# Kernel tuning notes

Measured on AMD Instinct MI355X. Metric: run time of the kernel, lower is better.

## Reference

```python
import jax, jax.numpy as jnp
import numpy as np


def setup_inputs() -> dict:
    key = jax.random.key(0)
    k1, k2 = jax.random.split(key)
    B, T, D = 32, 512, 512
    encoder_output = jax.random.normal(k1, (B, T, D), dtype=jnp.float32)
    durations = jax.random.randint(k2, (B, T), 0, 8, dtype=jnp.int32)
    return {"encoder_output": encoder_output, "durations": durations, "t_out": 4096}


def reference(encoder_output, durations, t_out):
    # Faithful to the TF loop: duration = max(dur, 1); repeat each phoneme
    # vector `duration` times along time; pad to fixed length t_out with zeros.
    B, T, D = encoder_output.shape
    dur = jnp.maximum(durations.astype(jnp.int32), 1)        # [B, T]
    ends = jnp.cumsum(dur, axis=1)                            # [B, T] cumulative end frame per phoneme
    pos = jnp.arange(t_out, dtype=jnp.int32)                  # [t_out] output frame indices
    # For frame j, source phoneme = first t with ends[t] > j  (searchsorted right)
    idx = jax.vmap(lambda e: jnp.searchsorted(e, pos, side='right'))(ends)  # [B, t_out]
    valid = pos[None, :] < ends[:, -1:]                       # frames past total length -> zero pad
    idx = jnp.minimum(idx, T - 1)
    out = jnp.take_along_axis(encoder_output, idx[:, :, None], axis=1)      # [B, t_out, D]
    return out * valid[:, :, None].astype(encoder_output.dtype)
```

## Files before the change

### kernel.cpp

```cpp
#include <hip/hip_runtime.h>


#define T_PH 512
#define FPB  8

typedef float f32x4 __attribute__((ext_vector_type(4)));

__global__ __launch_bounds__(256) void lr_fused_kernel(
    const f32x4* __restrict__ enc,
    const int*   __restrict__ dur,
    f32x4*       __restrict__ out,
    int T, int t_out) {

    __shared__ int sp[T_PH / 2];
    __shared__ int e[T_PH];
    __shared__ int idx8[FPB];

    const int tid = threadIdx.x;
    const int b   = blockIdx.y;
    const int j0  = blockIdx.x * FPB;

    int2 d2 = ((const int2*)(dur + b * T))[tid];
    int v0 = (d2.x < 1) ? 1 : d2.x;
    int v1 = (d2.y < 1) ? 1 : d2.y;
    sp[tid] = v0 + v1;
    __syncthreads();

    for (int off = 1; off < T_PH / 2; off <<= 1) {
        int add = (tid >= off) ? sp[tid - off] : 0;
        __syncthreads();
        sp[tid] += add;
        __syncthreads();
    }
    int S = sp[tid];
    e[2 * tid]     = S - v1;
    e[2 * tid + 1] = S;
    __syncthreads();

    const int total = e[T_PH - 1];

    if (tid < FPB) {
        int j = j0 + tid;
        int r;
        if (j >= total) {
            r = -1;
        } else {
            int lo = 0, hi = T_PH - 1;
            while (lo < hi) {
                int mid = (lo + hi) >> 1;
                if (e[mid] <= j) lo = mid + 1; else hi = mid;
            }
            r = lo;
        }
        idx8[tid] = r;
    }
    __syncthreads();

    const int lane = tid & 127;
    const int fh   = tid >> 7;

    const f32x4* __restrict__ encb = enc + (size_t)b * T_PH * 128;
    f32x4* __restrict__ outb = out + ((size_t)b * t_out + j0) * 128 + lane;

    const f32x4 zero = {0.f, 0.f, 0.f, 0.f};

    int p0 = idx8[fh + 0];
    int p1 = idx8[fh + 2];
    int p2 = idx8[fh + 4];
    int p3 = idx8[fh + 6];

    f32x4 w0 = (p0 >= 0) ? encb[(size_t)p0 * 128 + lane] : zero;
    f32x4 w1 = (p1 >= 0) ? encb[(size_t)p1 * 128 + lane] : zero;
    f32x4 w2 = (p2 >= 0) ? encb[(size_t)p2 * 128 + lane] : zero;
    f32x4 w3 = (p3 >= 0) ? encb[(size_t)p3 * 128 + lane] : zero;

    __builtin_nontemporal_store(w0, &outb[(size_t)(fh + 0) * 128]);
    __builtin_nontemporal_store(w1, &outb[(size_t)(fh + 2) * 128]);
    __builtin_nontemporal_store(w2, &outb[(size_t)(fh + 4) * 128]);
    __builtin_nontemporal_store(w3, &outb[(size_t)(fh + 6) * 128]);
}

extern "C" void kernel_launch(void* const* d_in, const int* in_sizes, int n_in,
                              void* d_out, int out_size, void* d_ws, size_t ws_size,
                              hipStream_t stream) {
    const float* enc = (const float*)d_in[0];
    const int* dur   = (const int*)d_in[1];
    float* out       = (float*)d_out;

    const int BT = in_sizes[1];
    const int T  = T_PH;
    const int B  = BT / T;
    const int D  = in_sizes[0] / BT;
    const int t_out = out_size / (B * D);

    dim3 grid(t_out / FPB, B);
    lr_fused_kernel<<<grid, 256, 0, stream>>>(
        (const f32x4*)enc, dur, (f32x4*)out, T, t_out);
}
```

Baseline: 52.02 us.

## Use wavefront shuffle scan and double frames per block

Replaces the shared-memory Hillis-Steele prefix sum, which needs many __syncthreads barriers, with a wave-level shuffle scan plus a small cross-wave combine. Doubles frames per block from 8 to 16, so each block's redundant duration scan is spread over twice as much output. This halves the grid, and each thread now issues eight gather loads and eight streaming stores instead of four, which raises register use.

```diff
diff --git a/kernel.cpp b/kernel.cpp
--- a/kernel.cpp
+++ b/kernel.cpp
@@ -2,7 +2,7 @@
 
 
 #define T_PH 512
-#define FPB  8
+#define FPB  16
 
 typedef float f32x4 __attribute__((ext_vector_type(4)));
 
@@ -10,29 +10,36 @@
     const f32x4* __restrict__ enc,
     const int*   __restrict__ dur,
     f32x4*       __restrict__ out,
-    int T, int t_out) {
+    int t_out) {
 
-    __shared__ int sp[T_PH / 2];
     __shared__ int e[T_PH];
-    __shared__ int idx8[FPB];
+    __shared__ int wtot[4];
+    __shared__ int idxs[FPB];
 
-    const int tid = threadIdx.x;
-    const int b   = blockIdx.y;
-    const int j0  = blockIdx.x * FPB;
+    const int tid  = threadIdx.x;
+    const int wav  = tid >> 6;
+    const int lane = tid & 63;
+    const int b    = blockIdx.y;
+    const int j0   = blockIdx.x * FPB;
 
-    int2 d2 = ((const int2*)(dur + b * T))[tid];
+    int2 d2 = ((const int2*)(dur + b * T_PH))[tid];
     int v0 = (d2.x < 1) ? 1 : d2.x;
     int v1 = (d2.y < 1) ? 1 : d2.y;
-    sp[tid] = v0 + v1;
+    int p  = v0 + v1;
+
+    #pragma unroll
+    for (int off = 1; off < 64; off <<= 1) {
+        int t = __shfl_up(p, off);
+        if (lane >= off) p += t;
+    }
+    if (lane == 63) wtot[wav] = p;
     __syncthreads();
 
-    for (int off = 1; off < T_PH / 2; off <<= 1) {
-        int add = (tid >= off) ? sp[tid - off] : 0;
-        __syncthreads();
-        sp[tid] += add;
-        __syncthreads();
-    }
-    int S = sp[tid];
+    int wbase = 0;
+    #pragma unroll
+    for (int w = 0; w < 3; ++w)
+        wbase += (wav > w) ? wtot[w] : 0;
+    int S = wbase + p;
     e[2 * tid]     = S - v1;
     e[2 * tid + 1] = S;
     __syncthreads();
@@ -52,32 +59,30 @@
             }
             r = lo;
         }
-        idx8[tid] = r;
+        idxs[tid] = r;
     }
     __syncthreads();
 
-    const int lane = tid & 127;
-    const int fh   = tid >> 7;
+    const int lane128 = tid & 127;
+    const int fh      = tid >> 7;
 
     const f32x4* __restrict__ encb = enc + (size_t)b * T_PH * 128;
-    f32x4* __restrict__ outb = out + ((size_t)b * t_out + j0) * 128 + lane;
+    f32x4* __restrict__ outb = out + ((size_t)b * t_out + j0) * 128 + lane128;
 
     const f32x4 zero = {0.f, 0.f, 0.f, 0.f};
 
-    int p0 = idx8[fh + 0];
-    int p1 = idx8[fh + 2];
-    int p2 = idx8[fh + 4];
-    int p3 = idx8[fh + 6];
+    int pi[8];
+    #pragma unroll
+    for (int k = 0; k < 8; ++k) pi[k] = idxs[fh + 2 * k];
 
-    f32x4 w0 = (p0 >= 0) ? encb[(size_t)p0 * 128 + lane] : zero;
-    f32x4 w1 = (p1 >= 0) ? encb[(size_t)p1 * 128 + lane] : zero;
-    f32x4 w2 = (p2 >= 0) ? encb[(size_t)p2 * 128 + lane] : zero;
-    f32x4 w3 = (p3 >= 0) ? encb[(size_t)p3 * 128 + lane] : zero;
+    f32x4 w[8];
+    #pragma unroll
+    for (int k = 0; k < 8; ++k)
+        w[k] = (pi[k] >= 0) ? encb[(size_t)pi[k] * 128 + lane128] : zero;
 
-    __builtin_nontemporal_store(w0, &outb[(size_t)(fh + 0) * 128]);
-    __builtin_nontemporal_store(w1, &outb[(size_t)(fh + 2) * 128]);
-    __builtin_nontemporal_store(w2, &outb[(size_t)(fh + 4) * 128]);
-    __builtin_nontemporal_store(w3, &outb[(size_t)(fh + 6) * 128]);
+    #pragma unroll
+    for (int k = 0; k < 8; ++k)
+        __builtin_nontemporal_store(w[k], &outb[(size_t)(fh + 2 * k) * 128]);
 }
 
 extern "C" void kernel_launch(void* const* d_in, const int* in_sizes, int n_in,
@@ -95,5 +100,5 @@
 
     dim3 grid(t_out / FPB, B);
     lr_fused_kernel<<<grid, 256, 0, stream>>>(
-        (const f32x4*)enc, dur, (f32x4*)out, T, t_out);
+        (const f32x4*)enc, dur, (f32x4*)out, t_out);
 }
```

New measurement: 54.10 us. 1.04x slower.
